# Performance work log

Hardware: AMD Instinct MI355X
Metric: run time of the kernel (lower is better)

The kernel has to match this reference:

```python
import jax, jax.numpy as jnp
import numpy as np

EPS = 1e-5

# ---------------- numpy-side hash/index precomputation ----------------

def _key(c):
    c = c.astype(np.int64) + 2  # shift so all coords >= 0
    return (c[..., 0] * 4096 + c[..., 1]) * 4096 + c[..., 2]

def _lookup(table_keys, query_keys):
    order = np.argsort(table_keys)
    sk = table_keys[order]
    pos = np.clip(np.searchsorted(sk, query_keys), 0, len(sk) - 1)
    found = sk[pos] == query_keys
    return np.where(found, order[pos], -1).astype(np.int64)

def setup_inputs() -> dict:
    N, C_IN, C_OUT, RES = 400_000, 32, 64, 1.0
    rng = np.random.default_rng(0)
    coords = rng.uniform(0.0, 100.0, (N, 3)).astype(np.float32)
    pf = rng.standard_normal((N, C_IN)).astype(np.float32)

    # initial_voxelize: unique voxel coords + point->voxel map
    vc = np.floor(coords / RES).astype(np.int64)
    uv, p2v_in = np.unique(vc, axis=0, return_inverse=True)
    p2v_in = p2v_in.reshape(-1)
    cnt_in = np.bincount(p2v_in, minlength=len(uv)).astype(np.float32)

    # strided conv output lattice (stride 2)
    ouv = np.unique(uv // 2, axis=0)
    ikeys, okeys = _key(uv), _key(ouv)

    # kernel-2 stride-2 conv map: input voxel at 2*out + off, off in {0,1}^3
    offs2 = np.array([[i, j, k] for i in (0, 1) for j in (0, 1) for k in (0, 1)], np.int64)
    conv_map = np.stack([_lookup(ikeys, _key(ouv * 2 + o)) for o in offs2], axis=1)

    # kernel-3 neighbor map on the output lattice
    offs3 = np.array([[i, j, k] for i in (-1, 0, 1) for j in (-1, 0, 1) for k in (-1, 0, 1)], np.int64)
    nbr27 = np.stack([_lookup(okeys, _key(ouv + o)) for o in offs3], axis=1)

    # trilinear voxel_to_point on output lattice (voxel size = 2*RES)
    q = coords / (2.0 * RES)
    base = np.floor(q).astype(np.int64)
    frac = (q - base).astype(np.float32)
    tri_idx, tri_w = [], []
    for o in offs2:
        idx = _lookup(okeys, _key(base + o))
        w = np.prod(np.where(o[None, :] == 1, frac, 1.0 - frac), axis=1).astype(np.float32)
        tri_idx.append(idx)
        tri_w.append(np.where(idx >= 0, w, 0.0).astype(np.float32))
    tri_idx = np.stack(tri_idx, axis=1)
    tri_w = np.stack(tri_w, axis=1)

    # point_to_voxel: containing output voxel (always exists)
    p2v_out = _lookup(okeys, _key(base))
    cnt_out = np.bincount(p2v_out, minlength=len(ouv)).astype(np.float32)

    def glorot(r, *shape):
        fan_in = shape[-2] * int(np.prod(shape[:-2])) if len(shape) > 2 else shape[0]
        return (r.standard_normal(shape) / np.sqrt(fan_in)).astype(np.float32)

    return dict(
        pf=jnp.asarray(pf),
        Wc=jnp.asarray(glorot(rng, 8, C_IN, C_OUT)),
        g1=jnp.ones(C_OUT, jnp.float32), b1=jnp.zeros(C_OUT, jnp.float32),
        Wr1=jnp.asarray(glorot(rng, 27, C_OUT, C_OUT)),
        gr1=jnp.ones(C_OUT, jnp.float32), br1=jnp.zeros(C_OUT, jnp.float32),
        Wr2=jnp.asarray(glorot(rng, 27, C_OUT, C_OUT)),
        gr2=jnp.ones(C_OUT, jnp.float32), br2=jnp.zeros(C_OUT, jnp.float32),
        Wpt=jnp.asarray(glorot(rng, C_OUT, C_OUT)), bpt=jnp.zeros(C_OUT, jnp.float32),
        gp=jnp.ones(C_OUT, jnp.float32), bp=jnp.zeros(C_OUT, jnp.float32),
        tri_w=jnp.asarray(tri_w), cnt_in=jnp.asarray(cnt_in), cnt_out=jnp.asarray(cnt_out),
        p2v_in=jnp.asarray(p2v_in), conv_map=jnp.asarray(conv_map),
        nbr27=jnp.asarray(nbr27), tri_idx=jnp.asarray(tri_idx), p2v_out=jnp.asarray(p2v_out),
    )

# ---------------- jax forward ----------------

def _bn(x, g, b):  # training-mode batch norm over voxel/point dim
    m = x.mean(0)
    v = x.var(0)
    return (x - m) * jax.lax.rsqrt(v + EPS) * g + b

def _seg_mean(x, seg, cnt):  # spvoxelize: scatter-mean
    return jax.ops.segment_sum(x, seg, num_segments=cnt.shape[0]) / cnt[:, None]

def _sconv(f, nbr, W):  # sparse conv: per-offset gather + matmul accumulate
    out = jnp.zeros((nbr.shape[0], W.shape[2]), f.dtype)
    for k in range(W.shape[0]):
        idx = nbr[:, k]
        g = jnp.where((idx >= 0)[:, None], f[jnp.maximum(idx, 0)], 0.0)
        out = out + g @ W[k]
    return out

def _tri(f, idx, w):  # trilinear voxel->point gather (w already 0 for missing)
    out = jnp.zeros((idx.shape[0], f.shape[1]), f.dtype)
    for j in range(idx.shape[1]):
        out = out + w[:, j:j + 1] * f[jnp.maximum(idx[:, j], 0)]
    return out

def reference(pf, Wc, g1, b1, Wr1, gr1, br1, Wr2, gr2, br2, Wpt, bpt, gp, bp,
              tri_w, cnt_in, cnt_out, p2v_in, conv_map, nbr27, tri_idx, p2v_out):
    vf0 = _seg_mean(pf, p2v_in, cnt_in)                         # initial_voxelize [M_in,32]
    vf1 = jax.nn.relu(_bn(_sconv(vf0, conv_map, Wc), g1, b1))   # conv_in [M_out,64]
    pfeat = _tri(vf1, tri_idx, tri_w)                           # voxel_to_point [N,64]
    vf2 = _seg_mean(pfeat, p2v_out, cnt_out)                    # point_to_voxel [M_out,64]
    h = jax.nn.relu(_bn(_sconv(vf2, nbr27, Wr1), gr1, br1))     # ResBlock conv1
    h = jax.nn.relu(_bn(_sconv(h, nbr27, Wr2), gr2, br2))       # ResBlock conv2
    vf3 = h + vf2                                               # residual sum
    p_out = jax.nn.relu(_bn(pfeat @ Wpt + bpt, gp, bp))         # point_layer
    pfeat2 = _tri(vf3, tri_idx, tri_w) + p_out                  # v2p + fuse
    vf4 = _seg_mean(pfeat2, p2v_out, cnt_out)                   # point_to_voxel
    return vf4, pfeat2
```

## Files before the change

kernel.cpp:

```cpp
#include <hip/hip_runtime.h>

#define EPSV 1e-5f
#define CDIV(a, b) (((a) + (b) - 1) / (b))

using short8 = __attribute__((ext_vector_type(8))) short;
using f32x4 = __attribute__((ext_vector_type(4))) float;

__device__ __forceinline__ unsigned short bf16rne(float x) {
  unsigned u = __float_as_uint(x);
  unsigned r = (u + 0x7fffu + ((u >> 16) & 1u)) >> 16;
  return (unsigned short)r;
}

__global__ void k_scatter_in(const float* __restrict__ pf, const int* __restrict__ p2v,
                             float* __restrict__ vf0, int total) {
  int i = blockIdx.x * 256 + threadIdx.x;
  if (i >= total) return;
  atomicAdd(&vf0[(size_t)p2v[i >> 5] * 32 + (i & 31)], pf[i]);
}

__global__ void k_div_in(float* __restrict__ vf0, const float* __restrict__ cnt, int total) {
  int i = blockIdx.x * 256 + threadIdx.x;
  if (i >= total) return;
  vf0[i] /= cnt[i >> 5];
}

__global__ __launch_bounds__(256) void k_conv1(const float* __restrict__ vin,
                                               const int* __restrict__ cmap,
                                               const float* __restrict__ W,
                                               float* __restrict__ out,
                                               float* __restrict__ stats, int Vout) {
  __shared__ float fs[32][128];
  __shared__ float Ws[32 * 64];
  __shared__ int idxs[128 * 8];
  __shared__ float ss[128];
  const int tid = threadIdx.x;
  const int vb = blockIdx.x * 128;
  for (int i = tid; i < 128 * 8; i += 256) {
    int g = vb * 8 + i;
    idxs[i] = (g < Vout * 8) ? cmap[g] : -1;
  }
  if (tid < 128) ss[tid] = 0.f;
  const int vq = tid & 15, cq = tid >> 4;
  const int v0 = vq * 8, c0 = cq * 4;
  const int srow = tid & 127, sci = (tid >> 7) * 16;
  float acc[8][4];
#pragma unroll
  for (int r = 0; r < 8; ++r)
#pragma unroll
    for (int q = 0; q < 4; ++q) acc[r][q] = 0.f;

  for (int k = 0; k < 8; ++k) {
    __syncthreads();
    for (int i = tid; i < 32 * 64; i += 256) Ws[i] = W[k * 2048 + i];
    int idx = idxs[srow * 8 + k];
    if (idx >= 0) {
#pragma unroll
      for (int j = 0; j < 16; j += 4) {
        float4 t = *(const float4*)&vin[(size_t)idx * 32 + sci + j];
        fs[sci + j + 0][srow] = t.x;
        fs[sci + j + 1][srow] = t.y;
        fs[sci + j + 2][srow] = t.z;
        fs[sci + j + 3][srow] = t.w;
      }
    } else {
#pragma unroll
      for (int j = 0; j < 16; ++j) fs[sci + j][srow] = 0.f;
    }
    __syncthreads();
#pragma unroll 8
    for (int ci = 0; ci < 32; ++ci) {
      float4 w4 = *(const float4*)&Ws[ci * 64 + c0];
      float4 fa = *(const float4*)&fs[ci][v0];
      float4 fb = *(const float4*)&fs[ci][v0 + 4];
      float fv[8] = {fa.x, fa.y, fa.z, fa.w, fb.x, fb.y, fb.z, fb.w};
      float wv[4] = {w4.x, w4.y, w4.z, w4.w};
#pragma unroll
      for (int r = 0; r < 8; ++r)
#pragma unroll
        for (int q = 0; q < 4; ++q) acc[r][q] += fv[r] * wv[q];
    }
  }
  float s1[4] = {0, 0, 0, 0}, s2[4] = {0, 0, 0, 0};
#pragma unroll
  for (int r = 0; r < 8; ++r) {
    int v = vb + v0 + r;
    if (v < Vout) {
      *(float4*)&out[(size_t)v * 64 + c0] =
          make_float4(acc[r][0], acc[r][1], acc[r][2], acc[r][3]);
#pragma unroll
      for (int q = 0; q < 4; ++q) {
        float x = acc[r][q];
        s1[q] += x;
        s2[q] += x * x;
      }
    }
  }
#pragma unroll
  for (int q = 0; q < 4; ++q) {
    atomicAdd(&ss[c0 + q], s1[q]);
    atomicAdd(&ss[64 + c0 + q], s2[q]);
  }
  __syncthreads();
  if (tid < 128) atomicAdd(&stats[tid], ss[tid]);
}

__global__ void k_bnfin(const float* __restrict__ stats, const float* __restrict__ g,
                        const float* __restrict__ b, float* __restrict__ sb, int rows) {
  int c = threadIdx.x;
  float inv = 1.f / (float)rows;
  float m = stats[c] * inv;
  float v = stats[64 + c] * inv - m * m;
  float sc = g[c] * rsqrtf(v + EPSV);
  sb[c] = sc;
  sb[64 + c] = b[c] - m * sc;
}

__global__ __launch_bounds__(1024) void k_scan_part(const float* __restrict__ cnt,
                                                    int* __restrict__ partial, int V) {
  __shared__ int s[1024];
  int i = blockIdx.x * 1024 + threadIdx.x;
  s[threadIdx.x] = (i < V) ? (int)cnt[i] : 0;
  __syncthreads();
  for (int st = 512; st > 0; st >>= 1) {
    if (threadIdx.x < st) s[threadIdx.x] += s[threadIdx.x + st];
    __syncthreads();
  }
  if (threadIdx.x == 0) partial[blockIdx.x] = s[0];
}

__global__ __launch_bounds__(1024) void k_scan_top(int* __restrict__ partial, int nb) {
  __shared__ int s[1024];
  int t = threadIdx.x;
  int orig = (t < nb) ? partial[t] : 0;
  s[t] = orig;
  __syncthreads();
  for (int st = 1; st < 1024; st <<= 1) {
    int v = (t >= st) ? s[t - st] : 0;
    __syncthreads();
    s[t] += v;
    __syncthreads();
  }
  if (t < nb) partial[t] = s[t] - orig;
}

__global__ __launch_bounds__(1024) void k_scan_write(const float* __restrict__ cnt,
                                                     const int* __restrict__ partial,
                                                     int* __restrict__ starts,
                                                     int* __restrict__ cursor, int V) {
  __shared__ int s[1024];
  int t = threadIdx.x;
  int i = blockIdx.x * 1024 + t;
  int orig = (i < V) ? (int)cnt[i] : 0;
  s[t] = orig;
  __syncthreads();
  for (int st = 1; st < 1024; st <<= 1) {
    int v = (t >= st) ? s[t - st] : 0;
    __syncthreads();
    s[t] += v;
    __syncthreads();
  }
  if (i < V) {
    int excl = s[t] - orig + partial[blockIdx.x];
    starts[i] = excl;
    cursor[i] = excl;
  }
}

__global__ void k_bucket(const int* __restrict__ p2v, int* __restrict__ cursor,
                         int* __restrict__ plist, int N) {
  int p = blockIdx.x * 256 + threadIdx.x;
  if (p >= N) return;
  int pos = atomicAdd(&cursor[p2v[p]], 1);
  plist[pos] = p;
}

__global__ __launch_bounds__(256) void k_tri1v(const float* __restrict__ c1,
                                               const float* __restrict__ sb0,
                                               const int* __restrict__ tidx,
                                               const float* __restrict__ twt,
                                               const int* __restrict__ starts,
                                               const float* __restrict__ cnt,
                                               const int* __restrict__ plist,
                                               float* __restrict__ pfeat,
                                               float* __restrict__ vf2, int V) {
  int t = threadIdx.x;
  int v = blockIdx.x * 4 + (t >> 6);
  int c = t & 63;
  if (v >= V) return;
  int s0 = starts[v];
  int n = (int)cnt[v];
  if (n < 1) return;
  int p0 = plist[s0];
  float sc = sb0[c], bi = sb0[64 + c];
  float R[8];
#pragma unroll
  for (int j = 0; j < 8; ++j) {
    int idx = tidx[(size_t)p0 * 8 + j];
    R[j] = (idx >= 0) ? fmaxf(sc * c1[(size_t)idx * 64 + c] + bi, 0.f) : 0.f;
  }
  float acc_v = 0.f;
  for (int i = 0; i < n; ++i) {
    int p = plist[s0 + i];
    float4 w0 = *(const float4*)&twt[(size_t)p * 8];
    float4 w1 = *(const float4*)&twt[(size_t)p * 8 + 4];
    float acc = w0.x * R[0] + w0.y * R[1] + w0.z * R[2] + w0.w * R[3] +
                w1.x * R[4] + w1.y * R[5] + w1.z * R[6] + w1.w * R[7];
    pfeat[(size_t)p * 64 + c] = acc;
    acc_v += acc;
  }
  vf2[(size_t)v * 64 + c] = acc_v / (float)n;
}

__global__ void k_wprep(const float* __restrict__ W, short* __restrict__ Wh,
                        short* __restrict__ Wl, int ntap) {
  int t = blockIdx.x * 256 + threadIdx.x;
  int total = ntap * 2 * 4 * 64;
  if (t >= total) return;
  int l = t & 63;
  int n = (t >> 6) & 3;
  int s = (t >> 8) & 1;
  int k = t >> 9;
  int co = n * 16 + (l & 15);
  int ci0 = s * 32 + (l >> 4) * 8;
#pragma unroll
  for (int j = 0; j < 8; ++j) {
    float x = W[((size_t)(k * 64 + ci0 + j)) * 64 + co];
    unsigned short hb = bf16rne(x);
    float hf = __uint_as_float((unsigned)hb << 16);
    Wh[(size_t)t * 8 + j] = (short)hb;
    Wl[(size_t)t * 8 + j] = (short)bf16rne(x - hf);
  }
}

__global__ void k_split(const float* __restrict__ in, const float* __restrict__ sb,
                        short* __restrict__ oh, short* __restrict__ ol, int total) {
  int i = blockIdx.x * 256 + threadIdx.x;
  if (i >= total) return;
  float x = in[i];
  if (sb) {
    int c = i & 63;
    x = fmaxf(sb[c] * x + sb[64 + c], 0.f);
  }
  unsigned short hb = bf16rne(x);
  float hf = __uint_as_float((unsigned)hb << 16);
  oh[i] = (short)hb;
  ol[i] = (short)bf16rne(x - hf);
}

__global__ __launch_bounds__(256) void k_conv27m(const short* __restrict__ Ah_g,
                                                 const short* __restrict__ Al_g,
                                                 const int* __restrict__ nbr,
                                                 const short* __restrict__ Wh,
                                                 const short* __restrict__ Wl,
                                                 float* __restrict__ out,
                                                 float* __restrict__ stats, int Vout) {
  __shared__ alignas(16) short As_h[1024 * 8];
  __shared__ alignas(16) short As_l[1024 * 8];
  __shared__ int idxs[128 * 27];
  __shared__ float ss[128];
  const int tid = threadIdx.x;
  const int vb = blockIdx.x * 128;
  for (int i = tid; i < 128 * 27; i += 256) {
    int g = vb * 27 + i;
    idxs[i] = (g < Vout * 27) ? nbr[g] : -1;
  }
  if (tid < 128) ss[tid] = 0.f;
  const int lane = tid & 63;
  const int w = tid >> 6;
  int sv[4], sj[4];
#pragma unroll
  for (int it = 0; it < 4; ++it) {
    int g = it * 256 + tid;
    sv[it] = ((g >> 7) << 4) | (g & 15);
    sj[it] = (g >> 4) & 7;
  }
  f32x4 acc[2][4];
#pragma unroll
  for (int m = 0; m < 2; ++m)
#pragma unroll
    for (int n = 0; n < 4; ++n)
#pragma unroll
      for (int r = 0; r < 4; ++r) acc[m][n][r] = 0.f;
  __syncthreads();

  uint4 rg[8];
#pragma unroll
  for (int it = 0; it < 8; ++it) {
    int idx = idxs[sv[it & 3] * 27 + 0];
    const short* src = (it < 4) ? Ah_g : Al_g;
    rg[it] = (idx >= 0) ? *(const uint4*)&src[(size_t)idx * 64 + sj[it & 3] * 8]
                        : make_uint4(0u, 0u, 0u, 0u);
  }
#pragma unroll
  for (int it = 0; it < 8; ++it) {
    int g = (it & 3) * 256 + tid;
    short* dst = (it < 4) ? As_h : As_l;
    *(uint4*)&dst[g * 8] = rg[it];
  }
  __syncthreads();

  for (int k = 0; k < 27; ++k) {
    if (k + 1 < 27) {
#pragma unroll
      for (int it = 0; it < 8; ++it) {
        int idx = idxs[sv[it & 3] * 27 + (k + 1)];
        const short* src = (it < 4) ? Ah_g : Al_g;
        rg[it] = (idx >= 0) ? *(const uint4*)&src[(size_t)idx * 64 + sj[it & 3] * 8]
                            : make_uint4(0u, 0u, 0u, 0u);
      }
    }
#pragma unroll
    for (int s = 0; s < 2; ++s) {
      short8 ah0 = *(const short8*)&As_h[((w * 4 + s) * 64 + lane) * 8];
      short8 al0 = *(const short8*)&As_l[((w * 4 + s) * 64 + lane) * 8];
      short8 ah1 = *(const short8*)&As_h[((w * 4 + 2 + s) * 64 + lane) * 8];
      short8 al1 = *(const short8*)&As_l[((w * 4 + 2 + s) * 64 + lane) * 8];
      const short* bph = Wh + ((size_t)(k * 2 + s) * 4) * 512;
      const short* bpl = Wl + ((size_t)(k * 2 + s) * 4) * 512;
#pragma unroll
      for (int n = 0; n < 4; ++n) {
        short8 bh = *(const short8*)&bph[n * 512 + lane * 8];
        short8 bl = *(const short8*)&bpl[n * 512 + lane * 8];
        acc[0][n] = __builtin_amdgcn_mfma_f32_16x16x32_bf16(ah0, bh, acc[0][n], 0, 0, 0);
        acc[0][n] = __builtin_amdgcn_mfma_f32_16x16x32_bf16(al0, bh, acc[0][n], 0, 0, 0);
        acc[0][n] = __builtin_amdgcn_mfma_f32_16x16x32_bf16(ah0, bl, acc[0][n], 0, 0, 0);
        acc[1][n] = __builtin_amdgcn_mfma_f32_16x16x32_bf16(ah1, bh, acc[1][n], 0, 0, 0);
        acc[1][n] = __builtin_amdgcn_mfma_f32_16x16x32_bf16(al1, bh, acc[1][n], 0, 0, 0);
        acc[1][n] = __builtin_amdgcn_mfma_f32_16x16x32_bf16(ah1, bl, acc[1][n], 0, 0, 0);
      }
    }
    __syncthreads();
    if (k + 1 < 27) {
#pragma unroll
      for (int it = 0; it < 8; ++it) {
        int g = (it & 3) * 256 + tid;
        short* dst = (it < 4) ? As_h : As_l;
        *(uint4*)&dst[g * 8] = rg[it];
      }
      __syncthreads();
    }
  }

  const int col = lane & 15, rq = lane >> 4;
#pragma unroll
  for (int m = 0; m < 2; ++m) {
#pragma unroll
    for (int n = 0; n < 4; ++n) {
      int c = n * 16 + col;
      float s1 = 0.f, s2 = 0.f;
#pragma unroll
      for (int r = 0; r < 4; ++r) {
        int v = vb + w * 32 + m * 16 + rq * 4 + r;
        if (v < Vout) {
          float x = acc[m][n][r];
          out[(size_t)v * 64 + c] = x;
          s1 += x;
          s2 += x * x;
        }
      }
      atomicAdd(&ss[c], s1);
      atomicAdd(&ss[64 + c], s2);
    }
  }
  __syncthreads();
  if (tid < 128) atomicAdd(&stats[tid], ss[tid]);
}

__global__ void k_vf3(const float* __restrict__ h2, const float* __restrict__ vf2,
                      const float* __restrict__ sb2, float* __restrict__ vf3, int total) {
  int i = blockIdx.x * 256 + threadIdx.x;
  if (i >= total) return;
  int c = i & 63;
  vf3[i] = fmaxf(sb2[c] * h2[i] + sb2[64 + c], 0.f) + vf2[i];
}

__global__ __launch_bounds__(256) void k_pmm(const float* __restrict__ pfeat,
                                             const float* __restrict__ Wpt,
                                             const float* __restrict__ bpt,
                                             float* __restrict__ outbuf,
                                             float* __restrict__ stats, int N) {
  __shared__ float fs[64][128];
  __shared__ float Ws[64 * 64];
  __shared__ float ss[128];
  const int tid = threadIdx.x;
  const int pb = blockIdx.x * 128;
  for (int i = tid; i < 64 * 64; i += 256) Ws[i] = Wpt[i];
  if (tid < 128) ss[tid] = 0.f;
  const int srow = tid & 127, sci = (tid >> 7) * 32;
  int p = pb + srow;
  if (p < N) {
#pragma unroll
    for (int j = 0; j < 32; j += 4) {
      float4 t = *(const float4*)&pfeat[(size_t)p * 64 + sci + j];
      fs[sci + j + 0][srow] = t.x;
      fs[sci + j + 1][srow] = t.y;
      fs[sci + j + 2][srow] = t.z;
      fs[sci + j + 3][srow] = t.w;
    }
  } else {
#pragma unroll
    for (int j = 0; j < 32; ++j) fs[sci + j][srow] = 0.f;
  }
  __syncthreads();
  const int vq = tid & 15, cq = tid >> 4;
  const int p0 = vq * 8, c0 = cq * 4;
  float acc[8][4];
#pragma unroll
  for (int r = 0; r < 8; ++r)
#pragma unroll
    for (int q = 0; q < 4; ++q) acc[r][q] = 0.f;
#pragma unroll 8
  for (int ci = 0; ci < 64; ++ci) {
    float4 w4 = *(const float4*)&Ws[ci * 64 + c0];
    float4 fa = *(const float4*)&fs[ci][p0];
    float4 fb = *(const float4*)&fs[ci][p0 + 4];
    float fv[8] = {fa.x, fa.y, fa.z, fa.w, fb.x, fb.y, fb.z, fb.w};
    float wv[4] = {w4.x, w4.y, w4.z, w4.w};
#pragma unroll
    for (int r = 0; r < 8; ++r)
#pragma unroll
      for (int q = 0; q < 4; ++q) acc[r][q] += fv[r] * wv[q];
  }
  float bb[4] = {bpt[c0], bpt[c0 + 1], bpt[c0 + 2], bpt[c0 + 3]};
  float s1[4] = {0, 0, 0, 0}, s2[4] = {0, 0, 0, 0};
#pragma unroll
  for (int r = 0; r < 8; ++r) {
    int pp = pb + p0 + r;
    if (pp < N) {
      float4 o;
      o.x = acc[r][0] + bb[0];
      o.y = acc[r][1] + bb[1];
      o.z = acc[r][2] + bb[2];
      o.w = acc[r][3] + bb[3];
      *(float4*)&outbuf[(size_t)pp * 64 + c0] = o;
      s1[0] += o.x; s2[0] += o.x * o.x;
      s1[1] += o.y; s2[1] += o.y * o.y;
      s1[2] += o.z; s2[2] += o.z * o.z;
      s1[3] += o.w; s2[3] += o.w * o.w;
    }
  }
#pragma unroll
  for (int q = 0; q < 4; ++q) {
    atomicAdd(&ss[c0 + q], s1[q]);
    atomicAdd(&ss[64 + c0 + q], s2[q]);
  }
  __syncthreads();
  if (tid < 128) atomicAdd(&stats[tid], ss[tid]);
}

__global__ __launch_bounds__(256) void k_tri2v(const float* __restrict__ vf3,
                                               const float* __restrict__ sb3,
                                               const int* __restrict__ tidx,
                                               const float* __restrict__ twt,
                                               const int* __restrict__ starts,
                                               const float* __restrict__ cnt,
                                               const int* __restrict__ plist,
                                               float* __restrict__ pf2,
                                               float* __restrict__ vf4, int V) {
  int t = threadIdx.x;
  int v = blockIdx.x * 4 + (t >> 6);
  int c = t & 63;
  if (v >= V) return;
  int s0 = starts[v];
  int n = (int)cnt[v];
  if (n < 1) return;
  int p0 = plist[s0];
  float S[8];
#pragma unroll
  for (int j = 0; j < 8; ++j) {
    int idx = tidx[(size_t)p0 * 8 + j];
    S[j] = (idx >= 0) ? vf3[(size_t)idx * 64 + c] : 0.f;
  }
  float s3 = sb3[c], b3 = sb3[64 + c];
  float acc_v = 0.f;
  for (int i = 0; i < n; ++i) {
    int p = plist[s0 + i];
    float4 w0 = *(const float4*)&twt[(size_t)p * 8];
    float4 w1 = *(const float4*)&twt[(size_t)p * 8 + 4];
    float raw = pf2[(size_t)p * 64 + c];
    float val = fmaxf(s3 * raw + b3, 0.f) +
                w0.x * S[0] + w0.y * S[1] + w0.z * S[2] + w0.w * S[3] +
                w1.x * S[4] + w1.y * S[5] + w1.z * S[6] + w1.w * S[7];
    pf2[(size_t)p * 64 + c] = val;
    acc_v += val;
  }
  vf4[(size_t)v * 64 + c] = acc_v / (float)n;
}

extern "C" void kernel_launch(void* const* d_in, const int* in_sizes, int n_in,
                              void* d_out, int out_size, void* d_ws, size_t ws_size,
                              hipStream_t stream) {
  const float* pf = (const float*)d_in[0];
  const float* Wc = (const float*)d_in[1];
  const float* g1 = (const float*)d_in[2];
  const float* b1 = (const float*)d_in[3];
  const float* Wr1 = (const float*)d_in[4];
  const float* gr1 = (const float*)d_in[5];
  const float* br1 = (const float*)d_in[6];
  const float* Wr2 = (const float*)d_in[7];
  const float* gr2 = (const float*)d_in[8];
  const float* br2 = (const float*)d_in[9];
  const float* Wpt = (const float*)d_in[10];
  const float* bpt = (const float*)d_in[11];
  const float* gp = (const float*)d_in[12];
  const float* bp = (const float*)d_in[13];
  const float* twt = (const float*)d_in[14];
  const float* cnt_in = (const float*)d_in[15];
  const float* cnt_out = (const float*)d_in[16];
  const int* p2v_in = (const int*)d_in[17];
  const int* conv_map = (const int*)d_in[18];
  const int* nbr27 = (const int*)d_in[19];
  const int* tri_idx = (const int*)d_in[20];
  const int* p2v_out = (const int*)d_in[21];

  const int N = in_sizes[0] / 32;
  const int Vin = in_sizes[15];
  const int Vout = in_sizes[16];

  float* ws = (float*)d_ws;
  size_t o = 0;
  auto alloc = [&](size_t nf) {
    float* pbase = ws + o;
    o += (nf + 63) & ~(size_t)63;
    return pbase;
  };
  size_t vf0_sz = (size_t)Vin * 32;
  size_t vf3_sz = (size_t)Vout * 64;
  float* vf0 = alloc(vf0_sz > vf3_sz ? vf0_sz : vf3_sz);
  float* c1 = alloc((size_t)Vout * 64);
  float* pfeat = alloc((size_t)N * 64);
  float* vf2 = alloc((size_t)Vout * 64);
  float* h1 = alloc((size_t)Vout * 64);
  float* stats = alloc(512);
  float* sb = alloc(512);
  int* partial = (int*)alloc(1024);
  int* starts = (int*)alloc(Vout);
  int* cursor = (int*)alloc(Vout);
  int* plist = (int*)alloc(N);
  const int WFRAG = 27 * 2 * 4 * 64 * 8;
  short* Wh1 = (short*)alloc(WFRAG / 2);
  short* Wl1 = (short*)alloc(WFRAG / 2);
  short* Wh2 = (short*)alloc(WFRAG / 2);
  short* Wl2 = (short*)alloc(WFRAG / 2);
  float* vf3 = vf0;
  float* h2 = c1;
  short* vf2h = (short*)pfeat;
  short* vf2l = vf2h + (size_t)Vout * 64;
  short* h1rh = vf2l + (size_t)Vout * 64;
  short* h1rl = h1rh + (size_t)Vout * 64;

  float* vf4 = (float*)d_out;
  float* pf2 = vf4 + (size_t)Vout * 64;

  const int nb = CDIV(Vout, 1024);

  hipMemsetAsync(vf0, 0, (size_t)Vin * 32 * sizeof(float), stream);
  hipMemsetAsync(stats, 0, 512 * sizeof(float), stream);

  k_scatter_in<<<CDIV(N * 32, 256), 256, 0, stream>>>(pf, p2v_in, vf0, N * 32);
  k_div_in<<<CDIV(Vin * 32, 256), 256, 0, stream>>>(vf0, cnt_in, Vin * 32);
  k_conv1<<<CDIV(Vout, 128), 256, 0, stream>>>(vf0, conv_map, Wc, c1, stats, Vout);
  k_bnfin<<<1, 64, 0, stream>>>(stats, g1, b1, sb, Vout);

  k_scan_part<<<nb, 1024, 0, stream>>>(cnt_out, partial, Vout);
  k_scan_top<<<1, 1024, 0, stream>>>(partial, nb);
  k_scan_write<<<nb, 1024, 0, stream>>>(cnt_out, partial, starts, cursor, Vout);
  k_bucket<<<CDIV(N, 256), 256, 0, stream>>>(p2v_out, cursor, plist, N);

  k_wprep<<<CDIV(27 * 2 * 4 * 64, 256), 256, 0, stream>>>(Wr1, Wh1, Wl1, 27);
  k_wprep<<<CDIV(27 * 2 * 4 * 64, 256), 256, 0, stream>>>(Wr2, Wh2, Wl2, 27);

  k_tri1v<<<CDIV(Vout, 4), 256, 0, stream>>>(c1, sb, tri_idx, twt, starts, cnt_out,
                                             plist, pfeat, vf2, Vout);

  k_pmm<<<CDIV(N, 128), 256, 0, stream>>>(pfeat, Wpt, bpt, pf2, stats + 384, N);
  k_bnfin<<<1, 64, 0, stream>>>(stats + 384, gp, bp, sb + 384, N);

  k_split<<<CDIV(Vout * 64, 256), 256, 0, stream>>>(vf2, nullptr, vf2h, vf2l, Vout * 64);
  k_conv27m<<<CDIV(Vout, 128), 256, 0, stream>>>(vf2h, vf2l, nbr27, Wh1, Wl1, h1,
                                                 stats + 128, Vout);
  k_bnfin<<<1, 64, 0, stream>>>(stats + 128, gr1, br1, sb + 128, Vout);

  k_split<<<CDIV(Vout * 64, 256), 256, 0, stream>>>(h1, sb + 128, h1rh, h1rl, Vout * 64);
  k_conv27m<<<CDIV(Vout, 128), 256, 0, stream>>>(h1rh, h1rl, nbr27, Wh2, Wl2, h2,
                                                 stats + 256, Vout);
  k_bnfin<<<1, 64, 0, stream>>>(stats + 256, gr2, br2, sb + 256, Vout);

  k_vf3<<<CDIV(Vout * 64, 256), 256, 0, stream>>>(h2, vf2, sb + 256, vf3, Vout * 64);

  k_tri2v<<<CDIV(Vout, 4), 256, 0, stream>>>(vf3, sb + 384, tri_idx, twt, starts,
                                             cnt_out, plist, pf2, vf4, Vout);
}
```

Measured before the change: 1.399 ms.

## Load conv27 A fragments directly from global into registers with packed hi/lo layout

Reworks the 27-neighbour sparse conv so each wavefront gathers its own MFMA A-operand fragments straight from global memory into registers, double-buffered across kernel offsets. This removes the LDS staging, the shared neighbour-index table and the per-offset block barriers. The bf16 hi/lo split is stored interleaved per voxel (128 shorts per row), so both halves sit in one contiguous row. The trade-off is more register pressure and less coalesced gathers, since each lane reads 16-byte chunks from scattered rows.

```diff
diff --git a/kernel.cpp b/kernel.cpp
--- a/kernel.cpp
+++ b/kernel.cpp
@@ -234,47 +234,36 @@
 }
 
 __global__ void k_split(const float* __restrict__ in, const float* __restrict__ sb,
-                        short* __restrict__ oh, short* __restrict__ ol, int total) {
+                        short* __restrict__ packed, int total) {
   int i = blockIdx.x * 256 + threadIdx.x;
   if (i >= total) return;
+  int c = i & 63;
   float x = in[i];
-  if (sb) {
-    int c = i & 63;
-    x = fmaxf(sb[c] * x + sb[64 + c], 0.f);
-  }
+  if (sb) x = fmaxf(sb[c] * x + sb[64 + c], 0.f);
   unsigned short hb = bf16rne(x);
   float hf = __uint_as_float((unsigned)hb << 16);
-  oh[i] = (short)hb;
-  ol[i] = (short)bf16rne(x - hf);
-}
-
-__global__ __launch_bounds__(256) void k_conv27m(const short* __restrict__ Ah_g,
-                                                 const short* __restrict__ Al_g,
+  size_t base = (size_t)(i >> 6) * 128 + c;
+  packed[base] = (short)hb;
+  packed[base + 64] = (short)bf16rne(x - hf);
+}
+
+__global__ __launch_bounds__(256) void k_conv27r(const short* __restrict__ A_g,
                                                  const int* __restrict__ nbr,
                                                  const short* __restrict__ Wh,
                                                  const short* __restrict__ Wl,
                                                  float* __restrict__ out,
                                                  float* __restrict__ stats, int Vout) {
-  __shared__ alignas(16) short As_h[1024 * 8];
-  __shared__ alignas(16) short As_l[1024 * 8];
-  __shared__ int idxs[128 * 27];
   __shared__ float ss[128];
   const int tid = threadIdx.x;
-  const int vb = blockIdx.x * 128;
-  for (int i = tid; i < 128 * 27; i += 256) {
-    int g = vb * 27 + i;
-    idxs[i] = (g < Vout * 27) ? nbr[g] : -1;
-  }
-  if (tid < 128) ss[tid] = 0.f;
   const int lane = tid & 63;
   const int w = tid >> 6;
-  int sv[4], sj[4];
-#pragma unroll
-  for (int it = 0; it < 4; ++it) {
-    int g = it * 256 + tid;
-    sv[it] = ((g >> 7) << 4) | (g & 15);
-    sj[it] = (g >> 4) & 7;
-  }
+  const int vb = blockIdx.x * 128 + w * 32;
+  if (tid < 128) ss[tid] = 0.f;
+  const int vv = lane & 15, kq = lane >> 4;
+  const int v0 = vb + vv, v1 = vb + 16 + vv;
+  const bool ok0 = v0 < Vout, ok1 = v1 < Vout;
+  const int koff = kq * 8;
+
   f32x4 acc[2][4];
 #pragma unroll
   for (int m = 0; m < 2; ++m)
@@ -282,46 +271,57 @@
     for (int n = 0; n < 4; ++n)
 #pragma unroll
       for (int r = 0; r < 4; ++r) acc[m][n][r] = 0.f;
-  __syncthreads();
-
-  uint4 rg[8];
-#pragma unroll
-  for (int it = 0; it < 8; ++it) {
-    int idx = idxs[sv[it & 3] * 27 + 0];
-    const short* src = (it < 4) ? Ah_g : Al_g;
-    rg[it] = (idx >= 0) ? *(const uint4*)&src[(size_t)idx * 64 + sj[it & 3] * 8]
-                        : make_uint4(0u, 0u, 0u, 0u);
-  }
-#pragma unroll
-  for (int it = 0; it < 8; ++it) {
-    int g = (it & 3) * 256 + tid;
-    short* dst = (it < 4) ? As_h : As_l;
-    *(uint4*)&dst[g * 8] = rg[it];
-  }
-  __syncthreads();
+
+  auto ldA = [&](int idx, int off) -> short8 {
+    if (idx < 0) {
+      short8 z = 0;
+      return z;
+    }
+    return *(const short8*)&A_g[(size_t)idx * 128 + off];
+  };
+
+  short8 cA[8], nA[8];
+  int idn0, idn1;
+
+  {
+    int i0 = ok0 ? nbr[(size_t)v0 * 27] : -1;
+    int i1 = ok1 ? nbr[(size_t)v1 * 27] : -1;
+#pragma unroll
+    for (int s = 0; s < 2; ++s)
+#pragma unroll
+      for (int h = 0; h < 2; ++h) {
+        cA[s * 2 + h] = ldA(i0, h * 64 + s * 32 + koff);
+        cA[4 + s * 2 + h] = ldA(i1, h * 64 + s * 32 + koff);
+      }
+    idn0 = ok0 ? nbr[(size_t)v0 * 27 + 1] : -1;
+    idn1 = ok1 ? nbr[(size_t)v1 * 27 + 1] : -1;
+  }
 
   for (int k = 0; k < 27; ++k) {
+    int idf0 = -1, idf1 = -1;
     if (k + 1 < 27) {
 #pragma unroll
-      for (int it = 0; it < 8; ++it) {
-        int idx = idxs[sv[it & 3] * 27 + (k + 1)];
-        const short* src = (it < 4) ? Ah_g : Al_g;
-        rg[it] = (idx >= 0) ? *(const uint4*)&src[(size_t)idx * 64 + sj[it & 3] * 8]
-                            : make_uint4(0u, 0u, 0u, 0u);
+      for (int s = 0; s < 2; ++s)
+#pragma unroll
+        for (int h = 0; h < 2; ++h) {
+          nA[s * 2 + h] = ldA(idn0, h * 64 + s * 32 + koff);
+          nA[4 + s * 2 + h] = ldA(idn1, h * 64 + s * 32 + koff);
+        }
+      if (k + 2 < 27) {
+        idf0 = ok0 ? nbr[(size_t)v0 * 27 + (k + 2)] : -1;
+        idf1 = ok1 ? nbr[(size_t)v1 * 27 + (k + 2)] : -1;
       }
     }
+    const short* bkh = Wh + (size_t)k * 4096 + lane * 8;
+    const short* bkl = Wl + (size_t)k * 4096 + lane * 8;
 #pragma unroll
     for (int s = 0; s < 2; ++s) {
-      short8 ah0 = *(const short8*)&As_h[((w * 4 + s) * 64 + lane) * 8];
-      short8 al0 = *(const short8*)&As_l[((w * 4 + s) * 64 + lane) * 8];
-      short8 ah1 = *(const short8*)&As_h[((w * 4 + 2 + s) * 64 + lane) * 8];
-      short8 al1 = *(const short8*)&As_l[((w * 4 + 2 + s) * 64 + lane) * 8];
-      const short* bph = Wh + ((size_t)(k * 2 + s) * 4) * 512;
-      const short* bpl = Wl + ((size_t)(k * 2 + s) * 4) * 512;
+      short8 ah0 = cA[s * 2], al0 = cA[s * 2 + 1];
+      short8 ah1 = cA[4 + s * 2], al1 = cA[4 + s * 2 + 1];
 #pragma unroll
       for (int n = 0; n < 4; ++n) {
-        short8 bh = *(const short8*)&bph[n * 512 + lane * 8];
-        short8 bl = *(const short8*)&bpl[n * 512 + lane * 8];
+        short8 bh = *(const short8*)&bkh[(s * 4 + n) * 512];
+        short8 bl = *(const short8*)&bkl[(s * 4 + n) * 512];
         acc[0][n] = __builtin_amdgcn_mfma_f32_16x16x32_bf16(ah0, bh, acc[0][n], 0, 0, 0);
         acc[0][n] = __builtin_amdgcn_mfma_f32_16x16x32_bf16(al0, bh, acc[0][n], 0, 0, 0);
         acc[0][n] = __builtin_amdgcn_mfma_f32_16x16x32_bf16(ah0, bl, acc[0][n], 0, 0, 0);
@@ -330,19 +330,16 @@
         acc[1][n] = __builtin_amdgcn_mfma_f32_16x16x32_bf16(ah1, bl, acc[1][n], 0, 0, 0);
       }
     }
-    __syncthreads();
     if (k + 1 < 27) {
 #pragma unroll
-      for (int it = 0; it < 8; ++it) {
-        int g = (it & 3) * 256 + tid;
-        short* dst = (it < 4) ? As_h : As_l;
-        *(uint4*)&dst[g * 8] = rg[it];
-      }
-      __syncthreads();
+      for (int q = 0; q < 8; ++q) cA[q] = nA[q];
+      idn0 = idf0;
+      idn1 = idf1;
     }
   }
 
   const int col = lane & 15, rq = lane >> 4;
+  __syncthreads();
 #pragma unroll
   for (int m = 0; m < 2; ++m) {
 #pragma unroll
@@ -351,7 +348,7 @@
       float s1 = 0.f, s2 = 0.f;
 #pragma unroll
       for (int r = 0; r < 4; ++r) {
-        int v = vb + w * 32 + m * 16 + rq * 4 + r;
+        int v = vb + m * 16 + rq * 4 + r;
         if (v < Vout) {
           float x = acc[m][n][r];
           out[(size_t)v * 64 + c] = x;
@@ -545,10 +542,8 @@
   short* Wl2 = (short*)alloc(WFRAG / 2);
   float* vf3 = vf0;
   float* h2 = c1;
-  short* vf2h = (short*)pfeat;
-  short* vf2l = vf2h + (size_t)Vout * 64;
-  short* h1rh = vf2l + (size_t)Vout * 64;
-  short* h1rl = h1rh + (size_t)Vout * 64;
+  short* vf2p = (short*)pfeat;
+  short* h1p = vf2p + (size_t)Vout * 128;
 
   float* vf4 = (float*)d_out;
   float* pf2 = vf4 + (size_t)Vout * 64;
@@ -577,13 +572,13 @@
   k_pmm<<<CDIV(N, 128), 256, 0, stream>>>(pfeat, Wpt, bpt, pf2, stats + 384, N);
   k_bnfin<<<1, 64, 0, stream>>>(stats + 384, gp, bp, sb + 384, N);
 
-  k_split<<<CDIV(Vout * 64, 256), 256, 0, stream>>>(vf2, nullptr, vf2h, vf2l, Vout * 64);
-  k_conv27m<<<CDIV(Vout, 128), 256, 0, stream>>>(vf2h, vf2l, nbr27, Wh1, Wl1, h1,
+  k_split<<<CDIV(Vout * 64, 256), 256, 0, stream>>>(vf2, nullptr, vf2p, Vout * 64);
+  k_conv27r<<<CDIV(Vout, 128), 256, 0, stream>>>(vf2p, nbr27, Wh1, Wl1, h1,
                                                  stats + 128, Vout);
   k_bnfin<<<1, 64, 0, stream>>>(stats + 128, gr1, br1, sb + 128, Vout);
 
-  k_split<<<CDIV(Vout * 64, 256), 256, 0, stream>>>(h1, sb + 128, h1rh, h1rl, Vout * 64);
-  k_conv27m<<<CDIV(Vout, 128), 256, 0, stream>>>(h1rh, h1rl, nbr27, Wh2, Wl2, h2,
+  k_split<<<CDIV(Vout * 64, 256), 256, 0, stream>>>(h1, sb + 128, h1p, Vout * 64);
+  k_conv27r<<<CDIV(Vout, 128), 256, 0, stream>>>(h1p, nbr27, Wh2, Wl2, h2,
                                                  stats + 256, Vout);
   k_bnfin<<<1, 64, 0, stream>>>(stats + 256, gr2, br2, sb + 256, Vout);
 
```

After: 1.236 ms. -11.7%, faster.
